# Kernel tuning notes

Hardware: AMD Instinct MI355X
Metric: run time of the kernel (lower is better)

The kernel has to match this reference:

```python
import jax, jax.numpy as jnp
import numpy as np

NUM_HEADS = 16


def _apply_rope(x, freqs):
    # x: (H, L, C), freqs: (L, C//2); computed in fp32, cast back to x.dtype
    xf = x.astype(jnp.float32)
    x1, x2 = jnp.split(xf, 2, axis=-1)
    f = freqs.astype(jnp.float32)[None]  # (1, L, C//2)
    cos, sin = jnp.cos(f), jnp.sin(f)
    out = jnp.concatenate((x1 * cos - x2 * sin, x1 * sin + x2 * cos), axis=-1)
    return out.astype(x.dtype)


def setup_inputs() -> dict:
    key = jax.random.key(0)
    k0, k1, k2, k3 = jax.random.split(key, 4)
    S, D, H = 4096, 1280, NUM_HEADS
    hd = D // H
    hidden_states = jax.random.normal(k0, (S, D), dtype=jnp.float32)
    cu_seqlens = jnp.array([0, 1024, 2048, 3072, 4096], dtype=jnp.int32)
    rotary_pos_emb = jax.random.normal(k1, (S, hd // 2), dtype=jnp.float32)
    scale = 1.0 / np.sqrt(D)
    w_qkv = (jax.random.normal(k2, (D, 3 * D), dtype=jnp.float32) * scale)
    b_qkv = jnp.zeros((3 * D,), dtype=jnp.float32)
    w_proj = (jax.random.normal(k3, (D, D), dtype=jnp.float32) * scale)
    b_proj = jnp.zeros((D,), dtype=jnp.float32)
    return {
        "hidden_states": hidden_states,
        "cu_seqlens": cu_seqlens,
        "rotary_pos_emb": rotary_pos_emb,
        "w_qkv": w_qkv,
        "b_qkv": b_qkv,
        "w_proj": w_proj,
        "b_proj": b_proj,
    }


def reference(hidden_states, cu_seqlens, rotary_pos_emb, w_qkv, b_qkv, w_proj, b_proj):
    S, D = hidden_states.shape
    H = NUM_HEADS
    hd = D // H
    qkv = hidden_states @ w_qkv + b_qkv            # (S, 3D)
    qkv = qkv.reshape(S, 3, H, hd).transpose(1, 2, 0, 3)  # (3, H, S, hd)
    q, k, v = qkv[0], qkv[1], qkv[2]
    q = _apply_rope(q, rotary_pos_emb)
    k = _apply_rope(k, rotary_pos_emb)
    # block-diagonal (per-segment) attention, equivalent to the per-segment loop
    seg = jnp.searchsorted(cu_seqlens, jnp.arange(S), side="right") - 1  # (S,)
    mask = seg[:, None] == seg[None, :]            # (S, S)
    scores = jnp.einsum("hqd,hkd->hqk", q, k) / np.sqrt(hd)
    scores = jnp.where(mask[None], scores, -jnp.inf)
    attn = jax.nn.softmax(scores.astype(jnp.float32), axis=-1).astype(q.dtype)
    out = jnp.einsum("hqk,hkd->qhd", attn, v).reshape(S, D)
    return out @ w_proj + b_proj
```

## Files before the change

### kernel.cpp

```cpp
#include <hip/hip_runtime.h>
#include <hip/hip_bf16.h>
#include <cstdint>

typedef __bf16 bf16x8 __attribute__((ext_vector_type(8)));
typedef __bf16 bf16x4 __attribute__((ext_vector_type(4)));
typedef short short4_ __attribute__((ext_vector_type(4)));
typedef float f32x4 __attribute__((ext_vector_type(4)));

#define SLEN 4096
#define DMODEL 1280
#define NHEADS 16
#define HD 80
#define HDP 96
#define VTILE_ELEMS 3328
#define VTILE_LDS 3584

#define GLD_LDS16(g, l)                                                        \
  __builtin_amdgcn_global_load_lds(                                            \
      (const __attribute__((address_space(1))) void*)(g),                      \
      (__attribute__((address_space(3))) void*)(l), 16, 0, 0)

#define WAIT_VMCNT(n) __builtin_amdgcn_s_waitcnt((n & 0xF) | 0x70 | 0xF00 | ((n >> 4) << 14))

#define FENCE asm volatile("" ::: "memory")
#define BARRIER do { FENCE; __builtin_amdgcn_s_barrier(); FENCE; } while (0)

__device__ __forceinline__ void transpose_body(const float* __restrict__ in,
                                               __bf16* __restrict__ out,
                                               int K, int N, int bx, int by, int t) {
  __shared__ float tile[32][33];
  int n0 = bx * 32, k0 = by * 32;
  int x = t & 31, y = t >> 5;
  for (int i = 0; i < 32; i += 8)
    tile[y + i][x] = in[(size_t)(k0 + y + i) * N + n0 + x];
  __syncthreads();
  for (int i = 0; i < 32; i += 8)
    out[(size_t)(n0 + y + i) * K + k0 + x] = (__bf16)tile[x][y + i];
}

__global__ __launch_bounds__(256) void prep(const float* __restrict__ hidden,
                                            __bf16* __restrict__ hid_b,
                                            const float* __restrict__ w_qkv,
                                            __bf16* __restrict__ wqkvT,
                                            const float* __restrict__ w_proj,
                                            __bf16* __restrict__ wprojT) {
  int bid = blockIdx.x, t = threadIdx.x;
  if (bid < 5120) {
    int i = bid * 256 + t;
    float4 v = ((const float4*)hidden)[i];
    bf16x4 o = { (__bf16)v.x, (__bf16)v.y, (__bf16)v.z, (__bf16)v.w };
    ((bf16x4*)hid_b)[i] = o;
  } else if (bid < 9920) {
    int b = bid - 5120;
    transpose_body(w_qkv, wqkvT, 1280, 3840, b % 120, b / 120, t);
  } else {
    int b = bid - 9920;
    transpose_body(w_proj, wprojT, 1280, 1280, b % 40, b / 40, t);
  }
}

template <int I0, int J0>
__device__ __forceinline__ void mfma16(f32x4 (&acc)[8][4], bf16x8 (&af)[4][2],
                                       bf16x8 (&bfr)[4][2]) {
  __builtin_amdgcn_s_setprio(1);
#pragma unroll
  for (int kk = 0; kk < 2; ++kk)
#pragma unroll
    for (int i = 0; i < 4; ++i)
#pragma unroll
      for (int j = 0; j < 2; ++j)
        acc[I0 + i][J0 + j] = __builtin_amdgcn_mfma_f32_16x16x32_bf16(
            bfr[J0 + j][kk], af[i][kk], acc[I0 + i][J0 + j], 0, 0, 0);
  __builtin_amdgcn_s_setprio(0);
}

__global__ __launch_bounds__(512, 2) void gemm256(const __bf16* __restrict__ A,
                                                  const __bf16* __restrict__ Bt,
                                                  const float* __restrict__ bias,
                                                  __bf16* __restrict__ C,
                                                  int M, int N, int K) {
  __shared__ __attribute__((aligned(1024))) __bf16 As[2][256 * 64];
  __shared__ __attribute__((aligned(1024))) __bf16 Bs[2][256 * 64];

  const int t = threadIdx.x;
  const int lane = t & 63, wave = t >> 6;
  const int quad = lane >> 4, l15 = lane & 15;
  const int wm = wave >> 2, wn = wave & 3;

  const int mb = M >> 8;
  const int cpx = gridDim.x >> 3;
  const int wg = (blockIdx.x & 7) * cpx + (blockIdx.x >> 3);
  const int bm = (wg % mb) * 256, bn = (wg / mb) * 256;

  const __bf16* Ab = A + (size_t)bm * K;
  const __bf16* Bb = Bt + (size_t)bn * K;

  auto stage = [&](const __bf16* g, __bf16* l, int row0, int kt) {
    GLD_LDS16(g + (size_t)(row0 + (lane >> 3)) * K + kt * 64 +
                  (((lane & 7) ^ ((lane >> 3) & 7)) << 3),
              l + row0 * 64);
  };
  auto lda = [&](bf16x8 (&dst)[4][2], const __bf16* Al, int I0) {
#pragma unroll
    for (int i = 0; i < 4; ++i)
#pragma unroll
      for (int kk = 0; kk < 2; ++kk) {
        int row = wm * 128 + (I0 + i) * 16 + l15;
        int c = (kk * 64 + quad * 16) ^ ((l15 & 7) << 4);
        dst[i][kk] = *(const bf16x8*)&Al[row * 64 + (c >> 1)];
      }
  };
  auto ldb = [&](bf16x8 (&dst)[2][2], const __bf16* Bl, int J0) {
#pragma unroll
    for (int j = 0; j < 2; ++j)
#pragma unroll
      for (int kk = 0; kk < 2; ++kk) {
        int row = wn * 64 + (J0 + j) * 16 + l15;
        int c = (kk * 64 + quad * 16) ^ ((l15 & 7) << 4);
        dst[j][kk] = *(const bf16x8*)&Bl[row * 64 + (c >> 1)];
      }
  };

  const int aw = wave * 8;
  const int be0 = (wave >> 2) * 64 + (wave & 3) * 8;
  const int niter = K >> 6;

  stage(Ab, As[0], aw, 0);        stage(Ab, As[0], 128 + aw, 0);
  stage(Bb, Bs[0], be0, 0);       stage(Bb, Bs[0], be0 + 128, 0);
  stage(Ab, As[0], 64 + aw, 0);   stage(Ab, As[0], 192 + aw, 0);
  stage(Bb, Bs[0], be0 + 32, 0);  stage(Bb, Bs[0], be0 + 160, 0);
  stage(Ab, As[1], aw, 1);        stage(Ab, As[1], 128 + aw, 1);
  stage(Bb, Bs[1], be0, 1);       stage(Bb, Bs[1], be0 + 128, 1);
  WAIT_VMCNT(4);
  BARRIER;

  f32x4 acc[8][4] = {};
  bf16x8 af[4][2], bfr[4][2];

  for (int it = 0; it < niter; ++it) {
    const int cur = it & 1;
    const __bf16* Ac = As[cur];
    const __bf16* Bc = Bs[cur];
    __bf16* An = As[cur ^ 1];
    __bf16* Bn = Bs[cur ^ 1];
    const bool p1 = it + 1 < niter, p2 = it + 2 < niter;

    lda(af, Ac, 0);
    ldb(reinterpret_cast<bf16x8(&)[2][2]>(bfr[0]), Bc, 0);
    if (p1) { stage(Ab, An, 64 + aw, it + 1); stage(Ab, An, 192 + aw, it + 1); }
    BARRIER;
    mfma16<0, 0>(acc, af, bfr);
    BARRIER;

    ldb(reinterpret_cast<bf16x8(&)[2][2]>(bfr[2]), Bc, 2);
    if (p1) { stage(Bb, Bn, be0 + 32, it + 1); stage(Bb, Bn, be0 + 160, it + 1); }
    BARRIER;
    mfma16<0, 2>(acc, af, bfr);
    BARRIER;

    lda(af, Ac, 4);
    if (p2) { stage(Ab, (__bf16*)Ac, aw, it + 2); stage(Ab, (__bf16*)Ac, 128 + aw, it + 2); }
    BARRIER;
    mfma16<4, 0>(acc, af, bfr);
    BARRIER;

    if (p2) { stage(Bb, (__bf16*)Bc, be0, it + 2); stage(Bb, (__bf16*)Bc, be0 + 128, it + 2); }
    BARRIER;
    mfma16<4, 2>(acc, af, bfr);
    if (p2) { WAIT_VMCNT(4); }
    else    { WAIT_VMCNT(0); }
    BARRIER;
  }

  float4 bv[4];
#pragma unroll
  for (int j = 0; j < 4; ++j)
    bv[j] = *(const float4*)&bias[bn + wn * 64 + j * 16 + quad * 4];
#pragma unroll
  for (int i = 0; i < 8; ++i) {
    size_t row = (size_t)(bm + wm * 128 + i * 16 + l15);
#pragma unroll
    for (int j = 0; j < 4; ++j) {
      int col = bn + wn * 64 + j * 16 + quad * 4;
      const float* bp = (const float*)&bv[j];
      bf16x4 ov;
#pragma unroll
      for (int r = 0; r < 4; ++r) ov[r] = (__bf16)(acc[i][j][r] + bp[r]);
      *(bf16x4*)&C[row * N + col] = ov;
    }
  }
}

template <int WMW>
__global__ __launch_bounds__(WMW * 2 * 64) void gemm_bt(const __bf16* __restrict__ A,
                                                        const __bf16* __restrict__ Bt,
                                                        const float* __restrict__ bias,
                                                        void* __restrict__ C,
                                                        int M, int N, int K, int store_bf16) {
  constexpr int BM = WMW * 64;
  constexpr int NW = WMW * 2;
  constexpr int BI = 8 / NW;
  constexpr int PW = 2 + BI;
  constexpr int ASZ = BM * 32, BSZ = 128 * 32;

  __shared__ __attribute__((aligned(16))) __bf16 As[3][ASZ];
  __shared__ __attribute__((aligned(16))) __bf16 Bs[3][BSZ];

  const int t = threadIdx.x;
  const int lane = t & 63, wave = t >> 6;
  const int quad = lane >> 4, l15 = lane & 15;
  const int wm = (wave & (WMW - 1)) * 64, wn = (wave / WMW) * 64;
  const int bm = blockIdx.x * BM, bn = blockIdx.y * 128;

  const int rs = lane >> 2, cs = (lane & 3) * 8;
  const __bf16* AgQ[2];
  const __bf16* BgQ[BI];
  int aLds[2], bLds[BI];
#pragma unroll
  for (int q = 0; q < 2; ++q) {
    int row = (wave * 2 + q) * 16;
    AgQ[q] = A + (size_t)(bm + row + rs) * K + cs;
    aLds[q] = row * 32;
  }
#pragma unroll
  for (int q = 0; q < BI; ++q) {
    int row = (wave * BI + q) * 16;
    BgQ[q] = Bt + (size_t)(bn + row + rs) * K + cs;
    bLds[q] = row * 32;
  }

  f32x4 acc[4][4] = {};
  const int niter = K >> 5;

#pragma unroll
  for (int s = 0; s < 2; ++s) {
#pragma unroll
    for (int q = 0; q < 2; ++q) GLD_LDS16(AgQ[q] + s * 32, &As[s][aLds[q]]);
#pragma unroll
    for (int q = 0; q < BI; ++q) GLD_LDS16(BgQ[q] + s * 32, &Bs[s][bLds[q]]);
  }

  int cmp = 0, stg = 2;
  for (int it = 0; it < niter; ++it) {
    const int kk = (it + 2 < niter ? it + 2 : niter - 1) * 32;
#pragma unroll
    for (int q = 0; q < 2; ++q) GLD_LDS16(AgQ[q] + kk, &As[stg][aLds[q]]);
#pragma unroll
    for (int q = 0; q < BI; ++q) GLD_LDS16(BgQ[q] + kk, &Bs[stg][bLds[q]]);
    asm volatile("" ::: "memory");
    WAIT_VMCNT(2 * PW);
    __builtin_amdgcn_s_barrier();
    asm volatile("" ::: "memory");

    bf16x8 af[4], bfr[4];
#pragma unroll
    for (int i = 0; i < 4; ++i)
      af[i] = *(const bf16x8*)&As[cmp][(wm + i * 16 + l15) * 32 + quad * 8];
#pragma unroll
    for (int j = 0; j < 4; ++j)
      bfr[j] = *(const bf16x8*)&Bs[cmp][(wn + j * 16 + l15) * 32 + quad * 8];
#pragma unroll
    for (int i = 0; i < 4; ++i)
#pragma unroll
      for (int j = 0; j < 4; ++j)
        acc[i][j] = __builtin_amdgcn_mfma_f32_16x16x32_bf16(bfr[j], af[i], acc[i][j], 0, 0, 0);

    asm volatile("" ::: "memory");
    __builtin_amdgcn_s_barrier();
    asm volatile("" ::: "memory");
    cmp = (cmp == 2) ? 0 : cmp + 1;
    stg = (stg == 2) ? 0 : stg + 1;
  }

  float4 bv[4];
#pragma unroll
  for (int j = 0; j < 4; ++j)
    bv[j] = *(const float4*)&bias[bn + wn + j * 16 + quad * 4];
#pragma unroll
  for (int i = 0; i < 4; ++i) {
    size_t row = (size_t)(bm + wm + i * 16 + l15);
#pragma unroll
    for (int j = 0; j < 4; ++j) {
      int col = bn + wn + j * 16 + quad * 4;
      const float* bp = (const float*)&bv[j];
      if (store_bf16) {
        bf16x4 ov;
#pragma unroll
        for (int r = 0; r < 4; ++r) ov[r] = (__bf16)(acc[i][j][r] + bp[r]);
        *(bf16x4*)&((__bf16*)C)[row * N + col] = ov;
      } else {
        float4 fv;
        fv.x = acc[i][j][0] + bp[0];
        fv.y = acc[i][j][1] + bp[1];
        fv.z = acc[i][j][2] + bp[2];
        fv.w = acc[i][j][3] + bp[3];
        *(float4*)&((float*)C)[row * N + col] = fv;
      }
    }
  }
}

__global__ __launch_bounds__(256) void rope_pack(const __bf16* __restrict__ qkv,
                                                 const float* __restrict__ freqs,
                                                 __bf16* __restrict__ qp,
                                                 __bf16* __restrict__ kp,
                                                 __bf16* __restrict__ vt) {
  const float QSCALE = 0.11180339887498949f * 1.44269504088896340f;
  int h = blockIdx.y;
  int s0 = blockIdx.x * 64;
  int t = threadIdx.x;
  int sp = t >> 2, l4 = t & 3;
  int s = s0 + sp;
  const __bf16* row = qkv + (size_t)s * 3840 + h * 80;
  __bf16* qo = qp + (size_t)(h * SLEN + s) * HDP;
  __bf16* ko = kp + (size_t)(h * SLEN + s) * HDP;

  __shared__ float vtile[64][81];

  for (int c = l4; c < 10; c += 4) {
    int base = (c < 5) ? c * 8 : (c - 5) * 8;
    bf16x8 xa = *(const bf16x8*)(row + base);
    bf16x8 xb = *(const bf16x8*)(row + base + 40);
    bf16x8 ya = *(const bf16x8*)(row + 1280 + base);
    bf16x8 yb = *(const bf16x8*)(row + 1280 + base + 40);
    float4 f0 = *(const float4*)(freqs + s * 40 + base);
    float4 f1 = *(const float4*)(freqs + s * 40 + base + 4);
    float fr[8] = {f0.x, f0.y, f0.z, f0.w, f1.x, f1.y, f1.z, f1.w};
    bf16x8 qv, kv;
#pragma unroll
    for (int e = 0; e < 8; ++e) {
      float cs = __builtin_cosf(fr[e]), sn = __builtin_sinf(fr[e]);
      float x1 = (float)xa[e], x2 = (float)xb[e];
      float y1 = (float)ya[e], y2 = (float)yb[e];
      float qvv, kvv;
      if (c < 5) { qvv = x1 * cs - x2 * sn; kvv = y1 * cs - y2 * sn; }
      else       { qvv = x1 * sn + x2 * cs; kvv = y1 * sn + y2 * cs; }
      qv[e] = (__bf16)(qvv * QSCALE);
      kv[e] = (__bf16)kvv;
    }
    *(bf16x8*)(qo + c * 8) = qv;
    *(bf16x8*)(ko + c * 8) = kv;
  }
  {
    bf16x8 z = {};
    if (l4 == 0) *(bf16x8*)(qo + 80) = z;
    if (l4 == 1) *(bf16x8*)(qo + 88) = z;
    if (l4 == 2) *(bf16x8*)(ko + 80) = z;
    if (l4 == 3) *(bf16x8*)(ko + 88) = z;
  }

  for (int c = l4; c < 10; c += 4) {
    bf16x8 v = *(const bf16x8*)(row + 2560 + c * 8);
#pragma unroll
    for (int e = 0; e < 8; ++e)
      vtile[sp][c * 8 + e] = (float)v[e];
  }
  __syncthreads();

  for (int idx = t; idx < 640; idx += 256) {
    int c2 = idx >= 320;
    int rem = idx - (c2 ? 320 : 0);
    int d = rem >> 2, kc = rem & 3;
    __bf16* tb = vt + (size_t)(h * (SLEN / 32) + (s0 >> 5) + c2) * VTILE_ELEMS;
    bf16x8 ov;
#pragma unroll
    for (int r = 0; r < 4; ++r) {
      ov[r]     = (__bf16)vtile[c2 * 32 + kc * 4 + r][d];
      ov[r + 4] = (__bf16)vtile[c2 * 32 + 16 + kc * 4 + r][d];
    }
    *(bf16x8*)(tb + d * 40 + kc * 8) = ov;
  }
}

__global__ __launch_bounds__(256) void flash_attn(const __bf16* __restrict__ qp,
                                                  const __bf16* __restrict__ kp,
                                                  const __bf16* __restrict__ vt,
                                                  const int* __restrict__ cu, int nseg,
                                                  __bf16* __restrict__ out) {
  const float MEXP = 16.0f;
  int h = blockIdx.y;
  int q0 = blockIdx.x * 128;
  int seg = 0;
  for (int i = 1; i < nseg; ++i)
    if (cu[i] <= q0) seg = i;
  int kstart = cu[seg], kend = cu[seg + 1];

  int t = threadIdx.x;
  int lane = t & 63, wave = t >> 6;
  int quad = lane >> 4, l15 = lane & 15;

  __shared__ __attribute__((aligned(16))) __bf16 Ks[2][64 * HDP];
  __shared__ __attribute__((aligned(16))) __bf16 Vs[2][2 * VTILE_LDS];

  bf16x8 qf[2][3];
#pragma unroll
  for (int qs = 0; qs < 2; ++qs) {
    const __bf16* qptr = qp + (size_t)(h * SLEN + q0 + wave * 32 + qs * 16 + l15) * HDP + quad * 8;
    qf[qs][0] = *(const bf16x8*)(qptr);
    qf[qs][1] = *(const bf16x8*)(qptr + 32);
    qf[qs][2] = *(const bf16x8*)(qptr + 64);
  }

  f32x4 o[2][5] = {};
  float l_p[2] = {0.f, 0.f};

  const __bf16* gK = kp + (size_t)(h * SLEN + kstart) * HDP + lane * 8;
  const __bf16* gV = vt + (size_t)(h * (SLEN / 32) + (kstart >> 5)) * VTILE_ELEMS + lane * 8;

  const int niter = (kend - kstart) >> 6;

  auto stage = [&](int kn, int buf) {
    const __bf16* ksrc = gK + (size_t)kn * (64 * HDP);
    const __bf16* vsrc = gV + (size_t)kn * (2 * VTILE_ELEMS);
#pragma unroll
    for (int i0 = 0; i0 < 7; ++i0) {
      int i = wave * 7 + i0;
      int ii = i < 26 ? i : 25;
      if (ii < 12)
        GLD_LDS16(ksrc + ii * 512, &Ks[buf][ii * 512]);
      else if (ii < 19)
        GLD_LDS16(vsrc + (ii - 12) * 512, &Vs[buf][(ii - 12) * 512]);
      else
        GLD_LDS16(vsrc + VTILE_ELEMS + (ii - 19) * 512, &Vs[buf][VTILE_LDS + (ii - 19) * 512]);
    }
  };

  stage(0, 0);

  for (int it = 0; it < niter; ++it) {
    const int cur = it & 1, nxt = cur ^ 1;
    const int kn = (it + 1 < niter) ? it + 1 : niter - 1;
    stage(kn, nxt);
    asm volatile("" ::: "memory");
    WAIT_VMCNT(7);
    __builtin_amdgcn_s_barrier();
    asm volatile("" ::: "memory");

    f32x4 sc[2][4];
#pragma unroll
    for (int nt = 0; nt < 4; ++nt) {
      sc[0][nt] = f32x4{-MEXP, -MEXP, -MEXP, -MEXP};
      sc[1][nt] = sc[0][nt];
#pragma unroll
      for (int c = 0; c < 3; ++c) {
        bf16x8 kf = *(const bf16x8*)&Ks[cur][(nt * 16 + l15) * HDP + quad * 8 + c * 32];
        sc[0][nt] = __builtin_amdgcn_mfma_f32_16x16x32_bf16(kf, qf[0][c], sc[0][nt], 0, 0, 0);
        sc[1][nt] = __builtin_amdgcn_mfma_f32_16x16x32_bf16(kf, qf[1][c], sc[1][nt], 0, 0, 0);
      }
    }

    bf16x4 pf[2][4];
#pragma unroll
    for (int qs = 0; qs < 2; ++qs)
#pragma unroll
      for (int nt = 0; nt < 4; ++nt)
#pragma unroll
        for (int r = 0; r < 4; ++r) {
          float p = __builtin_amdgcn_exp2f(sc[qs][nt][r]);
          l_p[qs] += p;
          pf[qs][nt][r] = (__bf16)p;
        }

#pragma unroll
    for (int g = 0; g < 2; ++g) {
      bf16x8 pc[2];
#pragma unroll
      for (int qs = 0; qs < 2; ++qs)
        pc[qs] = __builtin_shufflevector(pf[qs][g * 2], pf[qs][g * 2 + 1],
                                         0, 1, 2, 3, 4, 5, 6, 7);
#pragma unroll
      for (int dt = 0; dt < 5; ++dt) {
        bf16x8 vv = *(const bf16x8*)&Vs[cur][g * VTILE_LDS + (dt * 16 + l15) * 40 + quad * 8];
#pragma unroll
        for (int qs = 0; qs < 2; ++qs)
          o[qs][dt] = __builtin_amdgcn_mfma_f32_16x16x32_bf16(vv, pc[qs], o[qs][dt], 0, 0, 0);
      }
    }

    asm volatile("" ::: "memory");
    __builtin_amdgcn_s_barrier();
    asm volatile("" ::: "memory");
  }

#pragma unroll
  for (int qs = 0; qs < 2; ++qs) {
    float l = l_p[qs];
    l += __shfl_xor(l, 16);
    l += __shfl_xor(l, 32);
    float rinv = 1.0f / l;
    int qrow = q0 + wave * 32 + qs * 16 + l15;
#pragma unroll
    for (int dt = 0; dt < 5; ++dt) {
      bf16x4 ov;
#pragma unroll
      for (int r = 0; r < 4; ++r)
        ov[r] = (__bf16)(o[qs][dt][r] * rinv);
      *(bf16x4*)&out[(size_t)qrow * DMODEL + h * 80 + dt * 16 + quad * 4] = ov;
    }
  }
}

extern "C" void kernel_launch(void* const* d_in, const int* in_sizes, int n_in,
                              void* d_out, int out_size, void* d_ws, size_t ws_size,
                              hipStream_t stream) {
  const float* hidden = (const float*)d_in[0];
  const int* cu       = (const int*)d_in[1];
  const float* freqs  = (const float*)d_in[2];
  const float* w_qkv  = (const float*)d_in[3];
  const float* b_qkv  = (const float*)d_in[4];
  const float* w_proj = (const float*)d_in[5];
  const float* b_proj = (const float*)d_in[6];
  float* out = (float*)d_out;

  char* ws = (char*)d_ws;
  size_t off = 0;
  auto alloc = [&](size_t bytes) {
    char* p = ws + off;
    off += (bytes + 255) & ~(size_t)255;
    return p;
  };
  __bf16* hid_b  = (__bf16*)alloc((size_t)SLEN * DMODEL * 2);
  __bf16* wqkvT  = (__bf16*)alloc((size_t)3840 * 1280 * 2);
  __bf16* wprojT = (__bf16*)alloc((size_t)1280 * 1280 * 2);
  __bf16* qkvb   = (__bf16*)alloc((size_t)SLEN * 3840 * 2);
  __bf16* qp     = (__bf16*)alloc((size_t)NHEADS * SLEN * HDP * 2);
  __bf16* kp     = (__bf16*)alloc((size_t)NHEADS * SLEN * HDP * 2 + 1024);
  __bf16* vt     = (__bf16*)alloc((size_t)NHEADS * (SLEN / 32) * VTILE_ELEMS * 2 + 1024);
  __bf16* attn   = hid_b;

  prep<<<11520, 256, 0, stream>>>(hidden, hid_b, w_qkv, wqkvT, w_proj, wprojT);
  gemm256<<<dim3((SLEN / 256) * (3840 / 256)), 512, 0, stream>>>(hid_b, wqkvT, b_qkv, qkvb,
                                                                 SLEN, 3840, 1280);
  rope_pack<<<dim3(SLEN / 64, NHEADS), 256, 0, stream>>>(qkvb, freqs, qp, kp, vt);
  int nseg = in_sizes[1] - 1;
  flash_attn<<<dim3(SLEN / 128, NHEADS), 256, 0, stream>>>(qp, kp, vt, cu, nseg, attn);
  gemm_bt<2><<<dim3(SLEN / 128, DMODEL / 128), 256, 0, stream>>>(attn, wprojT, b_proj, out,
                                                                 SLEN, DMODEL, 1280, 0);
}
```

Measured before the change: 236.2 us.

## Replace output projection GEMM with swizzled, interleaved-pipeline 128x128 kernel

Replaces the generic gemm_bt used for the output projection with a new gemm128 kernel. It uses 64-wide K tiles with XOR-swizzled LDS layout, interleaves partial fragment loads, global-to-LDS staging and MFMA groups within each iteration, and remaps block indices for L2 locality. It also raises wave priority around MFMA blocks in both the GEMM and the flash attention kernel. The aim is to cut LDS bank conflicts and overlap memory with compute, at the cost of more barriers and more complex scheduling.

```diff
diff --git a/kernel.cpp b/kernel.cpp
--- a/kernel.cpp
+++ b/kernel.cpp
@@ -191,111 +191,140 @@
   }
 }
 
-template <int WMW>
-__global__ __launch_bounds__(WMW * 2 * 64) void gemm_bt(const __bf16* __restrict__ A,
-                                                        const __bf16* __restrict__ Bt,
-                                                        const float* __restrict__ bias,
-                                                        void* __restrict__ C,
-                                                        int M, int N, int K, int store_bf16) {
-  constexpr int BM = WMW * 64;
-  constexpr int NW = WMW * 2;
-  constexpr int BI = 8 / NW;
-  constexpr int PW = 2 + BI;
-  constexpr int ASZ = BM * 32, BSZ = 128 * 32;
-
-  __shared__ __attribute__((aligned(16))) __bf16 As[3][ASZ];
-  __shared__ __attribute__((aligned(16))) __bf16 Bs[3][BSZ];
+template <int I0, int J0>
+__device__ __forceinline__ void mfma8(f32x4 (&acc)[4][4], bf16x8 (&af)[2][2],
+                                      bf16x8 (&bfr)[4][2]) {
+  __builtin_amdgcn_s_setprio(1);
+#pragma unroll
+  for (int kk = 0; kk < 2; ++kk)
+#pragma unroll
+    for (int i = 0; i < 2; ++i)
+#pragma unroll
+      for (int j = 0; j < 2; ++j)
+        acc[I0 + i][J0 + j] = __builtin_amdgcn_mfma_f32_16x16x32_bf16(
+            bfr[J0 + j][kk], af[i][kk], acc[I0 + i][J0 + j], 0, 0, 0);
+  __builtin_amdgcn_s_setprio(0);
+}
+
+__global__ __launch_bounds__(256, 2) void gemm128(const __bf16* __restrict__ A,
+                                                  const __bf16* __restrict__ Bt,
+                                                  const float* __restrict__ bias,
+                                                  float* __restrict__ C,
+                                                  int M, int N, int K) {
+  __shared__ __attribute__((aligned(1024))) __bf16 As[2][128 * 64];
+  __shared__ __attribute__((aligned(1024))) __bf16 Bs[2][128 * 64];
 
   const int t = threadIdx.x;
   const int lane = t & 63, wave = t >> 6;
   const int quad = lane >> 4, l15 = lane & 15;
-  const int wm = (wave & (WMW - 1)) * 64, wn = (wave / WMW) * 64;
-  const int bm = blockIdx.x * BM, bn = blockIdx.y * 128;
-
-  const int rs = lane >> 2, cs = (lane & 3) * 8;
-  const __bf16* AgQ[2];
-  const __bf16* BgQ[BI];
-  int aLds[2], bLds[BI];
-#pragma unroll
-  for (int q = 0; q < 2; ++q) {
-    int row = (wave * 2 + q) * 16;
-    AgQ[q] = A + (size_t)(bm + row + rs) * K + cs;
-    aLds[q] = row * 32;
-  }
-#pragma unroll
-  for (int q = 0; q < BI; ++q) {
-    int row = (wave * BI + q) * 16;
-    BgQ[q] = Bt + (size_t)(bn + row + rs) * K + cs;
-    bLds[q] = row * 32;
-  }
+  const int wm = wave >> 1, wn = wave & 1;
+
+  const int mb = M >> 7;
+  const int cpx = gridDim.x >> 3;
+  const int wg = (blockIdx.x & 7) * cpx + (blockIdx.x >> 3);
+  const int bm = (wg % mb) * 128, bn = (wg / mb) * 128;
+
+  const __bf16* Ab = A + (size_t)bm * K;
+  const __bf16* Bb = Bt + (size_t)bn * K;
+
+  auto stage = [&](const __bf16* g, __bf16* l, int row0, int kt) {
+    GLD_LDS16(g + (size_t)(row0 + (lane >> 3)) * K + kt * 64 +
+                  (((lane & 7) ^ ((lane >> 3) & 7)) << 3),
+              l + row0 * 64);
+  };
+  auto lda2 = [&](bf16x8 (&dst)[2][2], const __bf16* Al, int I0) {
+#pragma unroll
+    for (int i = 0; i < 2; ++i)
+#pragma unroll
+      for (int kk = 0; kk < 2; ++kk) {
+        int row = wm * 64 + (I0 + i) * 16 + l15;
+        int c = (kk * 64 + quad * 16) ^ ((l15 & 7) << 4);
+        dst[i][kk] = *(const bf16x8*)&Al[row * 64 + (c >> 1)];
+      }
+  };
+  auto ldb2 = [&](bf16x8 (&dst)[2][2], const __bf16* Bl, int J0) {
+#pragma unroll
+    for (int j = 0; j < 2; ++j)
+#pragma unroll
+      for (int kk = 0; kk < 2; ++kk) {
+        int row = wn * 64 + (J0 + j) * 16 + l15;
+        int c = (kk * 64 + quad * 16) ^ ((l15 & 7) << 4);
+        dst[j][kk] = *(const bf16x8*)&Bl[row * 64 + (c >> 1)];
+      }
+  };
+
+  const int aw = wave * 8;
+  const int niter = K >> 6;
+
+  stage(Ab, As[0], aw, 0);        stage(Ab, As[0], 64 + aw, 0);
+  stage(Bb, Bs[0], aw, 0);        stage(Bb, Bs[0], 64 + aw, 0);
+  stage(Ab, As[0], 32 + aw, 0);   stage(Ab, As[0], 96 + aw, 0);
+  stage(Bb, Bs[0], 32 + aw, 0);   stage(Bb, Bs[0], 96 + aw, 0);
+  stage(Ab, As[1], aw, 1);        stage(Ab, As[1], 64 + aw, 1);
+  stage(Bb, Bs[1], aw, 1);        stage(Bb, Bs[1], 64 + aw, 1);
+  WAIT_VMCNT(4);
+  BARRIER;
 
   f32x4 acc[4][4] = {};
-  const int niter = K >> 5;
-
-#pragma unroll
-  for (int s = 0; s < 2; ++s) {
-#pragma unroll
-    for (int q = 0; q < 2; ++q) GLD_LDS16(AgQ[q] + s * 32, &As[s][aLds[q]]);
-#pragma unroll
-    for (int q = 0; q < BI; ++q) GLD_LDS16(BgQ[q] + s * 32, &Bs[s][bLds[q]]);
-  }
-
-  int cmp = 0, stg = 2;
+  bf16x8 af[2][2], bfr[4][2];
+
   for (int it = 0; it < niter; ++it) {
-    const int kk = (it + 2 < niter ? it + 2 : niter - 1) * 32;
-#pragma unroll
-    for (int q = 0; q < 2; ++q) GLD_LDS16(AgQ[q] + kk, &As[stg][aLds[q]]);
-#pragma unroll
-    for (int q = 0; q < BI; ++q) GLD_LDS16(BgQ[q] + kk, &Bs[stg][bLds[q]]);
-    asm volatile("" ::: "memory");
-    WAIT_VMCNT(2 * PW);
-    __builtin_amdgcn_s_barrier();
-    asm volatile("" ::: "memory");
-
-    bf16x8 af[4], bfr[4];
-#pragma unroll
-    for (int i = 0; i < 4; ++i)
-      af[i] = *(const bf16x8*)&As[cmp][(wm + i * 16 + l15) * 32 + quad * 8];
-#pragma unroll
-    for (int j = 0; j < 4; ++j)
-      bfr[j] = *(const bf16x8*)&Bs[cmp][(wn + j * 16 + l15) * 32 + quad * 8];
-#pragma unroll
-    for (int i = 0; i < 4; ++i)
-#pragma unroll
-      for (int j = 0; j < 4; ++j)
-        acc[i][j] = __builtin_amdgcn_mfma_f32_16x16x32_bf16(bfr[j], af[i], acc[i][j], 0, 0, 0);
-
-    asm volatile("" ::: "memory");
-    __builtin_amdgcn_s_barrier();
-    asm volatile("" ::: "memory");
-    cmp = (cmp == 2) ? 0 : cmp + 1;
-    stg = (stg == 2) ? 0 : stg + 1;
-  }
-
-  float4 bv[4];
+    const int cur = it & 1;
+    const __bf16* Ac = As[cur];
+    const __bf16* Bc = Bs[cur];
+    __bf16* An = As[cur ^ 1];
+    __bf16* Bn = Bs[cur ^ 1];
+    const bool p1 = it + 1 < niter, p2 = it + 2 < niter;
+
+    lda2(af, Ac, 0);
+    ldb2(reinterpret_cast<bf16x8(&)[2][2]>(bfr[0]), Bc, 0);
+    if (p1) { stage(Ab, An, 32 + aw, it + 1); stage(Ab, An, 96 + aw, it + 1); }
+    BARRIER;
+    mfma8<0, 0>(acc, af, bfr);
+    BARRIER;
+
+    ldb2(reinterpret_cast<bf16x8(&)[2][2]>(bfr[2]), Bc, 2);
+    if (p1) { stage(Bb, Bn, 32 + aw, it + 1); stage(Bb, Bn, 96 + aw, it + 1); }
+    BARRIER;
+    mfma8<0, 2>(acc, af, bfr);
+    BARRIER;
+
+    lda2(af, Ac, 2);
+    if (p2) { stage(Ab, (__bf16*)Ac, aw, it + 2); stage(Ab, (__bf16*)Ac, 64 + aw, it + 2); }
+    BARRIER;
+    mfma8<2, 0>(acc, af, bfr);
+    BARRIER;
+
+    if (p2) { stage(Bb, (__bf16*)Bc, aw, it + 2); stage(Bb, (__bf16*)Bc, 64 + aw, it + 2); }
+    BARRIER;
+    mfma8<2, 2>(acc, af, bfr);
+    if (p2) { WAIT_VMCNT(4); }
+    else    { WAIT_VMCNT(0); }
+    BARRIER;
+  }
+
+  float4 bv[2];
+#pragma unroll
+  for (int j = 0; j < 2; ++j)
+    bv[j] = *(const float4*)&bias[bn + wn * 64 + (2 * 0 + j) * 16 + quad * 4];
+  float4 bv4[4];
 #pragma unroll
   for (int j = 0; j < 4; ++j)
-    bv[j] = *(const float4*)&bias[bn + wn + j * 16 + quad * 4];
+    bv4[j] = *(const float4*)&bias[bn + wn * 64 + j * 16 + quad * 4];
+  (void)bv;
 #pragma unroll
   for (int i = 0; i < 4; ++i) {
-    size_t row = (size_t)(bm + wm + i * 16 + l15);
+    size_t row = (size_t)(bm + wm * 64 + i * 16 + l15);
 #pragma unroll
     for (int j = 0; j < 4; ++j) {
-      int col = bn + wn + j * 16 + quad * 4;
-      const float* bp = (const float*)&bv[j];
-      if (store_bf16) {
-        bf16x4 ov;
-#pragma unroll
-        for (int r = 0; r < 4; ++r) ov[r] = (__bf16)(acc[i][j][r] + bp[r]);
-        *(bf16x4*)&((__bf16*)C)[row * N + col] = ov;
-      } else {
-        float4 fv;
-        fv.x = acc[i][j][0] + bp[0];
-        fv.y = acc[i][j][1] + bp[1];
-        fv.z = acc[i][j][2] + bp[2];
-        fv.w = acc[i][j][3] + bp[3];
-        *(float4*)&((float*)C)[row * N + col] = fv;
-      }
+      int col = bn + wn * 64 + j * 16 + quad * 4;
+      const float* bp = (const float*)&bv4[j];
+      float4 fv;
+      fv.x = acc[i][j][0] + bp[0];
+      fv.y = acc[i][j][1] + bp[1];
+      fv.z = acc[i][j][2] + bp[2];
+      fv.w = acc[i][j][3] + bp[3];
+      *(float4*)&C[row * N + col] = fv;
     }
   }
 }
@@ -437,6 +466,7 @@
     asm volatile("" ::: "memory");
 
     f32x4 sc[2][4];
+    __builtin_amdgcn_s_setprio(1);
 #pragma unroll
     for (int nt = 0; nt < 4; ++nt) {
       sc[0][nt] = f32x4{-MEXP, -MEXP, -MEXP, -MEXP};
@@ -448,6 +478,7 @@
         sc[1][nt] = __builtin_amdgcn_mfma_f32_16x16x32_bf16(kf, qf[1][c], sc[1][nt], 0, 0, 0);
       }
     }
+    __builtin_amdgcn_s_setprio(0);
 
     bf16x4 pf[2][4];
 #pragma unroll
@@ -461,6 +492,7 @@
           pf[qs][nt][r] = (__bf16)p;
         }
 
+    __builtin_amdgcn_s_setprio(1);
 #pragma unroll
     for (int g = 0; g < 2; ++g) {
       bf16x8 pc[2];
@@ -476,6 +508,7 @@
           o[qs][dt] = __builtin_amdgcn_mfma_f32_16x16x32_bf16(vv, pc[qs], o[qs][dt], 0, 0, 0);
       }
     }
+    __builtin_amdgcn_s_setprio(0);
 
     asm volatile("" ::: "memory");
     __builtin_amdgcn_s_barrier();
@@ -534,6 +567,6 @@
   rope_pack<<<dim3(SLEN / 64, NHEADS), 256, 0, stream>>>(qkvb, freqs, qp, kp, vt);
   int nseg = in_sizes[1] - 1;
   flash_attn<<<dim3(SLEN / 128, NHEADS), 256, 0, stream>>>(qp, kp, vt, cu, nseg, attn);
-  gemm_bt<2><<<dim3(SLEN / 128, DMODEL / 128), 256, 0, stream>>>(attn, wprojT, b_proj, out,
-                                                                 SLEN, DMODEL, 1280, 0);
-}
+  gemm128<<<dim3((SLEN / 128) * (DMODEL / 128)), 256, 0, stream>>>(attn, wprojT, b_proj, out,
+                                                                   SLEN, DMODEL, 1280);
+}
```

Result: faster. 229.8 us (-2.7%).
